# Kernel optimization log

Hardware: AMD Instinct MI355X
Metric: run time of the kernel (lower is better)

The kernel has to match this reference:

```python
import jax, jax.numpy as jnp
import numpy as np
from jax import lax

EPS = 1e-5  # torch BatchNorm default eps

# Binarization with straight-through estimator (hard-tanh gradient window),
# matching BinaryFunc in dizcza/MCMC_BinaryNet.
@jax.custom_vjp
def binarize(x):
    return jnp.sign(x)

def _bin_fwd(x):
    return jnp.sign(x), x

def _bin_bwd(res, g):
    return (g * (jnp.abs(res) <= 1.0).astype(g.dtype),)

binarize.defvjp(_bin_fwd, _bin_bwd)

def bn2d(x, gamma, beta):
    # training-mode BatchNorm2d: batch stats over (N,H,W), biased variance
    m = x.mean(axis=(0, 2, 3), keepdims=True)
    v = x.var(axis=(0, 2, 3), keepdims=True)
    xn = (x - m) * lax.rsqrt(v + EPS)
    return xn * gamma[None, :, None, None] + beta[None, :, None, None]

def bn1d(x, gamma, beta):
    m = x.mean(axis=0, keepdims=True)
    v = x.var(axis=0, keepdims=True)
    return (x - m) * lax.rsqrt(v + EPS) * gamma[None, :] + beta[None, :]

def bconv(x, w):
    # BinaryDecorator(Conv2d): sign(x) conv sign(W), padding=0, no bias
    return lax.conv_general_dilated(binarize(x), binarize(w), (1, 1), 'VALID',
                                    dimension_numbers=('NCHW', 'OIHW', 'NCHW'))

def maxpool2(x):
    return lax.reduce_window(x, -jnp.inf, lax.max, (1, 1, 2, 2), (1, 1, 2, 2), 'VALID')

def prelu(x, a):
    return jnp.where(x >= 0, x, a * x)


def setup_inputs() -> dict:
    key = jax.random.key(0)
    ks = iter(jax.random.split(key, 16))
    conv_channels = [3, 128, 256, 512]
    fc_sizes = [512 * 6 * 6, 1024, 10]
    d = {'x': jax.random.normal(next(ks), (128, 3, 64, 64), jnp.float32)}
    for i, (cin, cout) in enumerate(zip(conv_channels[:-1], conv_channels[1:])):
        d[f'cg{i}'] = jnp.ones((cin,), jnp.float32)          # BN2d gamma
        d[f'cb{i}'] = jnp.zeros((cin,), jnp.float32)         # BN2d beta
        d[f'cw{i}'] = jax.random.normal(next(ks), (cout, cin, 3, 3), jnp.float32) * 0.05
        d[f'cp{i}'] = jnp.full((1,), 0.25, jnp.float32)      # PReLU (num_parameters=1)
    for i, (fin, fout) in enumerate(zip(fc_sizes[:-1], fc_sizes[1:])):
        d[f'fg{i}'] = jnp.ones((fin,), jnp.float32)
        d[f'fb{i}'] = jnp.zeros((fin,), jnp.float32)
        d[f'fw{i}'] = jax.random.normal(next(ks), (fout, fin), jnp.float32) * 0.05
        d[f'fp{i}'] = jnp.full((1,), 0.25, jnp.float32)
    d['scale'] = jnp.full((1,), 1e-3, jnp.float32)           # ScaleLayer init
    return d


def reference(x, cg0, cb0, cw0, cp0, cg1, cb1, cw1, cp1, cg2, cb2, cw2, cp2,
              fg0, fb0, fw0, fp0, fg1, fb1, fw1, fp1, scale):
    for cg, cb, cw, cp in ((cg0, cb0, cw0, cp0), (cg1, cb1, cw1, cp1), (cg2, cb2, cw2, cp2)):
        x = bn2d(x, cg, cb)
        x = bconv(x, cw)
        x = maxpool2(x)
        x = prelu(x, cp)
    x = x.reshape(x.shape[0], -1)  # [B, 512*6*6]
    for fg, fb, fw, fp in ((fg0, fb0, fw0, fp0), (fg1, fb1, fw1, fp1)):
        x = bn1d(x, fg, fb)
        x = binarize(x) @ binarize(fw).T  # BinaryDecorator(Linear), no bias
        x = prelu(x, fp)
    return x * scale
```

## Files before the change

### kernel.cpp

```cpp
#include <hip/hip_runtime.h>
#include <cstdint>
#include <cstddef>

#define BN_EPS 1e-5


__global__ void zero_d(double* p, int n) {
  int i = blockIdx.x * blockDim.x + threadIdx.x;
  if (i < n) p[i] = 0.0;
}

__global__ void reduce_plane(const float* __restrict__ x, double* __restrict__ sums,
                             int C, int HW) {
  int c = blockIdx.x, n = blockIdx.y;
  const float* p = x + ((long)n * C + c) * HW;
  double s = 0.0, s2 = 0.0;
  for (int i = threadIdx.x; i < HW; i += blockDim.x) {
    double v = (double)p[i];
    s += v; s2 += v * v;
  }
  for (int o = 32; o > 0; o >>= 1) {
    s  += __shfl_down(s, o, 64);
    s2 += __shfl_down(s2, o, 64);
  }
  __shared__ double ls[4], ls2[4];
  int lane = threadIdx.x & 63, w = threadIdx.x >> 6;
  if (lane == 0) { ls[w] = s; ls2[w] = s2; }
  __syncthreads();
  if (threadIdx.x == 0) {
    double a = 0, b = 0;
    for (int i = 0; i < 4; i++) { a += ls[i]; b += ls2[i]; }
    atomicAdd(&sums[2 * c], a);
    atomicAdd(&sums[2 * c + 1], b);
  }
}

__global__ void reduce_cl(const float* __restrict__ x, double* __restrict__ sums,
                          int C, long rows) {
  int lane = threadIdx.x & 63, wv = threadIdx.x >> 6;
  int c = blockIdx.x * 64 + lane;
  double s = 0.0, s2 = 0.0;
  for (long r = blockIdx.y * 4 + wv; r < rows; r += (long)gridDim.y * 4) {
    double v = (double)x[r * C + c];
    s += v; s2 += v * v;
  }
  __shared__ double ls[4][64], ls2[4][64];
  ls[wv][lane] = s; ls2[wv][lane] = s2;
  __syncthreads();
  if (threadIdx.x < 64) {
    double a = ls[0][lane] + ls[1][lane] + ls[2][lane] + ls[3][lane];
    double b = ls2[0][lane] + ls2[1][lane] + ls2[2][lane] + ls2[3][lane];
    atomicAdd(&sums[2 * c], a);
    atomicAdd(&sums[2 * c + 1], b);
  }
}

__global__ void reduce_cols2(const float* __restrict__ x, double* __restrict__ sums,
                             int R, int F, int RS) {
  int f = blockIdx.x * blockDim.x + threadIdx.x;
  int r0 = blockIdx.y * RS, r1 = min(r0 + RS, R);
  double s = 0.0, s2 = 0.0;
  for (int r = r0; r < r1; r++) {
    double v = (double)x[(long)r * F + f];
    s += v; s2 += v * v;
  }
  atomicAdd(&sums[2 * f], s);
  atomicAdd(&sums[2 * f + 1], s2);
}

__global__ void finalize_stats(const double* __restrict__ sums, double2* __restrict__ st,
                               int C, double cnt) {
  int c = blockIdx.x * blockDim.x + threadIdx.x;
  if (c >= C) return;
  double m = sums[2 * c] / cnt;
  double v = sums[2 * c + 1] / cnt - m * m;
  st[c] = make_double2(m, 1.0 / sqrt(v + BN_EPS));
}


__global__ void pack_bits_c1(const float* __restrict__ x, const double2* __restrict__ st,
                             const float* __restrict__ g, const float* __restrict__ b,
                             uint64_t* __restrict__ rows) {
  int wid = blockIdx.x * 4 + (threadIdx.x >> 6);
  int lane = threadIdx.x & 63;
  int n = wid / 192, rem = wid % 192;
  int ci = rem >> 6, y = rem & 63;
  double2 s = st[ci];
  float xv = x[(((long)n * 3 + ci) * 64 + y) * 64 + lane];
  float xn = (float)(((double)xv - s.x) * s.y) * g[ci] + b[ci];
  uint64_t m = __ballot(xn > 0.f);
  if (lane == 0) rows[wid] = m;
}

__global__ void pack_wc1(const float* __restrict__ w, uint32_t* __restrict__ wm) {
  int co = threadIdx.x;
  uint32_t m = 0;
  for (int j = 0; j < 27; j++) m |= (uint32_t)(w[co * 27 + j] > 0.f) << j;
  wm[co] = m;
}

__global__ void pack_cl(const float* __restrict__ acl, const double2* __restrict__ st,
                        const float* __restrict__ g, const float* __restrict__ b,
                        uint64_t* __restrict__ out, int C, long nwords, int lw) {
  long wid = (long)blockIdx.x * 4 + (threadIdx.x >> 6);
  if (wid >= nwords) return;
  int lane = threadIdx.x & 63;
  long row = wid >> lw;
  int w = (int)(wid & ((1 << lw) - 1));
  int c = w * 64 + lane;
  double2 s = st[c];
  float xv = acl[row * C + c];
  float xn = (float)(((double)xv - s.x) * s.y) * g[c] + b[c];
  uint64_t m = __ballot(xn > 0.f);
  if (lane == 0) out[wid] = m;
}

__global__ void pack_wconv(const float* __restrict__ w, uint64_t* __restrict__ out,
                           int CO, int CI, int W) {
  int i = blockIdx.x * blockDim.x + threadIdx.x;
  int total = CO * 9 * W;
  if (i >= total) return;
  int wd = i % W;
  int t = i / W;
  int tap = t % 9, co = t / 9;
  uint64_t bits = 0;
  for (int k = 0; k < 64; k++) {
    int ci = wd * 64 + k;
    bits |= (uint64_t)(w[((long)co * CI + ci) * 9 + tap] > 0.f) << k;
  }
  out[i] = bits;
}

__global__ void pack_nz(const float* __restrict__ x, const double2* __restrict__ st,
                        const float* __restrict__ g, const float* __restrict__ b,
                        uint64_t* __restrict__ out, int R, int F) {
  int Wf = F >> 6;
  long wid = (long)blockIdx.x * 4 + (threadIdx.x >> 6);
  if (wid >= (long)R * Wf) return;
  int lane = threadIdx.x & 63;
  long r = wid / Wf;
  int w = (int)(wid % Wf);
  int f = w * 64 + lane;
  double2 s = st[f];
  double d = (double)x[r * F + f] - s.x;
  float xn = (float)(d * s.y) * g[f] + b[f];
  uint64_t sm = __ballot(xn > 0.f);
  uint64_t nm = __ballot(d != 0.0);
  if (lane == 0) { out[2 * wid] = sm; out[2 * wid + 1] = nm; }
}

__global__ void pack_wfc2(const float* __restrict__ w, uint64_t* __restrict__ out,
                          int O, int F) {
  int Wf = F >> 6;
  long wid = (long)blockIdx.x * 4 + (threadIdx.x >> 6);
  if (wid >= (long)O * Wf) return;
  int lane = threadIdx.x & 63;
  long o = wid / Wf;
  int wd = (int)(wid % Wf);
  uint64_t m = __ballot(w[o * F + wd * 64 + lane] > 0.f);
  if (lane == 0) out[wid] = m;
}


__global__ __launch_bounds__(256) void conv1_pool3(const uint64_t* __restrict__ rows,
                                                   const uint32_t* __restrict__ wm,
                                                   const float* __restrict__ cp,
                                                   float* __restrict__ out) {
  __shared__ uint64_t rL[192];
  __shared__ uint32_t wL[128];
  __shared__ uint32_t mL[61 * 4];
  int n = blockIdx.y, chunk = blockIdx.x, t = threadIdx.x;
  if (t < 192) rL[t] = rows[n * 192 + t];
  if (t < 128) wL[t] = wm[t];
  __syncthreads();
  if (t < 244) {
    int pl = t >> 2, quad = t & 3;
    int pos = chunk * 61 + pl;
    if (pos < 961) {
      int py = pos / 31, px = pos - py * 31;
      int cy = 2 * py + (quad >> 1), cx = 2 * px + (quad & 1);
      uint32_t m = 0;
#pragma unroll
      for (int ci = 0; ci < 3; ci++)
#pragma unroll
        for (int ky = 0; ky < 3; ky++)
          m |= (uint32_t)((rL[ci * 64 + cy + ky] >> cx) & 7) << (ci * 9 + ky * 3);
      mL[pl * 4 + quad] = m;
    }
  }
  __syncthreads();
  int co = t & 127, slot = t >> 7;
  float alpha = cp[0];
  uint32_t w = wL[co];
  for (int i = slot; i < 61; i += 2) {
    int pos = chunk * 61 + i;
    if (pos >= 961) break;
    int p0 = __popc(mL[4 * i] ^ w);
    int p1 = __popc(mL[4 * i + 1] ^ w);
    int p2 = __popc(mL[4 * i + 2] ^ w);
    int p3 = __popc(mL[4 * i + 3] ^ w);
    int dot = 27 - 2 * min(min(p0, p1), min(p2, p3));
    float f = (float)dot;
    out[((long)n * 961 + pos) * 128 + co] = dot >= 0 ? f : alpha * f;
  }
}

template <int W, int IH>
__device__ __forceinline__ void load_half(uint64_t (&h)[4][2 * W],
                                          const uint64_t* __restrict__ sIn,
                                          int py, int cx) {
#pragma unroll
  for (int cy = 0; cy < 4; cy++) {
    const uint64_t* p = &sIn[((2 * py + cy) * IH + cx) * W];
#pragma unroll
    for (int i = 0; i < 2 * W; i++) h[cy][i] = p[i];
  }
}

template <int W>
__device__ __forceinline__ void conv_quad(const uint64_t (&A)[4][2 * W],
                                          const uint64_t (&B)[4][2 * W],
                                          const uint64_t (&wr)[9 * W],
                                          int& a00, int& a01, int& a10, int& a11) {
  a00 = a01 = a10 = a11 = 0;
#pragma unroll
  for (int cy = 0; cy < 4; cy++) {
#pragma unroll
    for (int dy = 0; dy < 2; dy++) {
      int ky = cy - dy;
      if (ky < 0 || ky > 2) continue;
#pragma unroll
      for (int dx = 0; dx < 2; dx++) {
        int acc = 0;
#pragma unroll
        for (int kx = 0; kx < 3; kx++) {
          int col = dx + kx;
#pragma unroll
          for (int wd = 0; wd < W; wd++) {
            uint64_t pv = (col < 2) ? A[cy][col * W + wd] : B[cy][(col - 2) * W + wd];
            acc += __popcll(pv ^ wr[(ky * 3 + kx) * W + wd]);
          }
        }
        if (dy == 0) { if (dx == 0) a00 += acc; else a01 += acc; }
        else         { if (dx == 0) a10 += acc; else a11 += acc; }
      }
    }
  }
}

template <int W, int IH, int PH, int CHUNK>
__global__ __attribute__((amdgpu_flat_work_group_size(256, 256),
                          amdgpu_waves_per_eu(2, 3)))
void convp_slide(
    const uint64_t* __restrict__ in, const uint64_t* __restrict__ wt,
    const float* __restrict__ cp, float* __restrict__ out, int CO) {
  __shared__ uint64_t sIn[10 * IH * W];
  int n = blockIdx.y;
  int cg = blockIdx.x / CHUNK, chunk = blockIdx.x % CHUNK;
  int t = threadIdx.x, lane = t & 63, slot = t >> 6;
  int r0 = chunk * 8;
  int nr = min(10, IH - r0);
  const uint64_t* src = in + ((long)n * IH + r0) * (IH * W);
  for (int i = t; i < nr * IH * W; i += 256) sIn[i] = src[i];
  int co = cg * 64 + lane;
  uint64_t wr[9 * W];
  const uint64_t* wg = wt + (long)co * (9 * W);
#pragma unroll
  for (int i = 0; i < 9 * W; i++) wr[i] = wg[i];
  __syncthreads();
  int py = chunk * 4 + slot;
  if (py >= PH) return;
  float alpha = cp[0];
  const int K = 9 * 64 * W;
  uint64_t hA[4][2 * W], hB[4][2 * W];
  load_half<W, IH>(hA, sIn, slot, 0);
#pragma unroll
  for (int px = 0; px < PH; px += 2) {
    load_half<W, IH>(hB, sIn, slot, 2 * px + 2);
    {
      int a00, a01, a10, a11;
      conv_quad<W>(hA, hB, wr, a00, a01, a10, a11);
      int dot = K - 2 * min(min(a00, a01), min(a10, a11));
      float f = (float)dot;
      out[((long)n * PH * PH + py * PH + px) * CO + co] = dot >= 0 ? f : alpha * f;
    }
    if (px + 1 < PH) {
      load_half<W, IH>(hA, sIn, slot, 2 * px + 4);
      int a00, a01, a10, a11;
      conv_quad<W>(hB, hA, wr, a00, a01, a10, a11);
      int dot = K - 2 * min(min(a00, a01), min(a10, a11));
      float f = (float)dot;
      out[((long)n * PH * PH + py * PH + px + 1) * CO + co] = dot >= 0 ? f : alpha * f;
    }
  }
}

template <int W, int IH, int PH, int POSCH, bool CL>
__global__ __attribute__((amdgpu_flat_work_group_size(256, 256),
                          amdgpu_waves_per_eu(2, 3)))
void convp_pool3(
    const uint64_t* __restrict__ in, const uint64_t* __restrict__ wt,
    const float* __restrict__ cp, float* __restrict__ out, int CO) {
  __shared__ uint64_t sIn[IH * IH * W];
  int n = blockIdx.y;
  int cg = blockIdx.x / POSCH;
  int chunk = blockIdx.x % POSCH;
  int t = threadIdx.x;
  const uint64_t* src = in + (long)n * (IH * IH * W);
  for (int i = t; i < IH * IH * W; i += 256) sIn[i] = src[i];
  int lane = t & 63;
  int slot = t >> 6;
  int co = cg * 64 + lane;
  uint64_t wr[9 * W];
  const uint64_t* wg = wt + (long)co * (9 * W);
#pragma unroll
  for (int i = 0; i < 9 * W; i++) wr[i] = wg[i];
  __syncthreads();
  float alpha = cp[0];
  for (int pos = chunk * 4 + slot; pos < PH * PH; pos += POSCH * 4) {
    int py = pos / PH, px = pos % PH;
    int a00 = 0, a01 = 0, a10 = 0, a11 = 0;
#pragma unroll
    for (int cy = 0; cy < 4; cy++) {
      uint64_t row[4 * W];
      const uint64_t* rp = &sIn[((2 * py + cy) * IH + 2 * px) * W];
#pragma unroll
      for (int i = 0; i < 4 * W; i++) row[i] = rp[i];
#pragma unroll
      for (int dy = 0; dy < 2; dy++) {
        int ky = cy - dy;
        if (ky < 0 || ky > 2) continue;
#pragma unroll
        for (int dx = 0; dx < 2; dx++) {
          int a = 0;
#pragma unroll
          for (int kx = 0; kx < 3; kx++)
#pragma unroll
            for (int wd = 0; wd < W; wd++)
              a += __popcll(row[(dx + kx) * W + wd] ^ wr[(ky * 3 + kx) * W + wd]);
          if (dy == 0) { if (dx == 0) a00 += a; else a01 += a; }
          else         { if (dx == 0) a10 += a; else a11 += a; }
        }
      }
    }
    int pmin = min(min(a00, a01), min(a10, a11));
    int dot = 9 * 64 * W - 2 * pmin;
    float f = (float)dot;
    long idx = CL ? (((long)n * PH * PH + pos) * CO + co)
                  : (((long)n * CO + co) * PH * PH + pos);
    out[idx] = dot >= 0 ? f : alpha * f;
  }
}


__global__ void fc_bin(const uint64_t* __restrict__ xp, const uint64_t* __restrict__ wp,
                       const float* __restrict__ cp, float* __restrict__ out,
                       int O, int Wf) {
  __shared__ uint64_t xs[288], xz[288];
  int r = blockIdx.y;
  for (int i = threadIdx.x; i < Wf; i += blockDim.x) {
    xs[i] = xp[((long)r * Wf + i) * 2];
    xz[i] = xp[((long)r * Wf + i) * 2 + 1];
  }
  __syncthreads();
  int o = blockIdx.x * blockDim.x + threadIdx.x;
  if (o >= O) return;
  int pc = 0, nzc = 0;
  const uint64_t* wr = wp + (long)o * Wf;
  for (int wd = 0; wd < Wf; wd++) {
    uint64_t nz = xz[wd];
    pc  += __popcll((xs[wd] ^ wr[wd]) & nz);
    nzc += __popcll(nz);
  }
  int dot = nzc - 2 * pc;
  float f = (float)dot;
  float alpha = cp[0];
  out[(long)r * O + o] = dot >= 0 ? f : alpha * f;
}

__global__ void fc_bin_scale(const uint64_t* __restrict__ xp, const uint64_t* __restrict__ wp,
                             const float* __restrict__ cp, const float* __restrict__ scale,
                             float* __restrict__ out, int R, int O, int Wf) {
  int i = blockIdx.x * blockDim.x + threadIdx.x;
  if (i >= R * O) return;
  int o = i % O, r = i / O;
  int pc = 0, nzc = 0;
  for (int wd = 0; wd < Wf; wd++) {
    uint64_t nz = xp[((long)r * Wf + wd) * 2 + 1];
    pc  += __popcll((xp[((long)r * Wf + wd) * 2] ^ wp[(long)o * Wf + wd]) & nz);
    nzc += __popcll(nz);
  }
  int dot = nzc - 2 * pc;
  float f = (float)dot;
  float alpha = cp[0];
  f = dot >= 0 ? f : alpha * f;
  out[i] = f * scale[0];
}


extern "C" void kernel_launch(void* const* d_in, const int* in_sizes, int n_in,
                              void* d_out, int out_size, void* d_ws, size_t ws_size,
                              hipStream_t stream) {
  const float* x   = (const float*)d_in[0];
  const float* cg0 = (const float*)d_in[1];
  const float* cb0 = (const float*)d_in[2];
  const float* cw0 = (const float*)d_in[3];
  const float* cp0 = (const float*)d_in[4];
  const float* cg1 = (const float*)d_in[5];
  const float* cb1 = (const float*)d_in[6];
  const float* cw1 = (const float*)d_in[7];
  const float* cp1 = (const float*)d_in[8];
  const float* cg2 = (const float*)d_in[9];
  const float* cb2 = (const float*)d_in[10];
  const float* cw2 = (const float*)d_in[11];
  const float* cp2 = (const float*)d_in[12];
  const float* fg0 = (const float*)d_in[13];
  const float* fb0 = (const float*)d_in[14];
  const float* fw0 = (const float*)d_in[15];
  const float* fp0 = (const float*)d_in[16];
  const float* fg1 = (const float*)d_in[17];
  const float* fb1 = (const float*)d_in[18];
  const float* fw1 = (const float*)d_in[19];
  const float* fp1 = (const float*)d_in[20];
  const float* scl = (const float*)d_in[21];

  char* ws = (char*)d_ws;
  size_t off = 0;
  auto alloc = [&](size_t bytes) {
    size_t r = off;
    off += (bytes + 255) & ~(size_t)255;
    return r;
  };
  const int C0_OFF = 0, C1_OFF = 16, C2_OFF = 160, C3_OFF = 448, C4_OFF = 18944;
  const int NCH = 19968;

  double*   sums  = (double*)(ws + alloc((size_t)NCH * 2 * sizeof(double)));
  double2*  stats = (double2*)(ws + alloc((size_t)NCH * sizeof(double2)));
  uint64_t* rows0 = (uint64_t*)(ws + alloc(128L * 3 * 64 * 8));
  uint32_t* wm1   = (uint32_t*)(ws + alloc(128L * 4));
  float*    a1    = (float*)(ws + alloc(128L * 961 * 128 * 4));
  uint64_t* s1p   = (uint64_t*)(ws + alloc(128L * 961 * 2 * 8));
  uint64_t* w1p   = (uint64_t*)(ws + alloc(256L * 9 * 2 * 8));
  float*    a2    = (float*)(ws + alloc(128L * 196 * 256 * 4));
  uint64_t* s2p   = (uint64_t*)(ws + alloc(128L * 196 * 4 * 8));
  uint64_t* w2p   = (uint64_t*)(ws + alloc(512L * 9 * 4 * 8));
  float*    a3    = (float*)(ws + alloc(128L * 512 * 36 * 4));
  uint64_t* s3p   = (uint64_t*)(ws + alloc(128L * 288 * 2 * 8));
  uint64_t* w3p   = (uint64_t*)(ws + alloc(1024L * 288 * 8));
  float*    f1    = (float*)(ws + alloc(128L * 1024 * 4));
  uint64_t* s4p   = (uint64_t*)(ws + alloc(128L * 16 * 2 * 8));
  uint64_t* w4p   = (uint64_t*)(ws + alloc(10L * 16 * 8));

  const int B = 256;

  zero_d<<<dim3(156), B, 0, stream>>>(sums, NCH * 2);

  reduce_plane<<<dim3(3, 128), B, 0, stream>>>(x, sums + 2 * C0_OFF, 3, 4096);
  finalize_stats<<<1, 64, 0, stream>>>(sums + 2 * C0_OFF, stats + C0_OFF, 3, 524288.0);
  pack_bits_c1<<<dim3(6144), B, 0, stream>>>(x, stats + C0_OFF, cg0, cb0, rows0);
  pack_wc1<<<1, 128, 0, stream>>>(cw0, wm1);
  conv1_pool3<<<dim3(16, 128), B, 0, stream>>>(rows0, wm1, cp0, a1);

  reduce_cl<<<dim3(2, 256), B, 0, stream>>>(a1, sums + 2 * C1_OFF, 128, 123008L);
  finalize_stats<<<1, 128, 0, stream>>>(sums + 2 * C1_OFF, stats + C1_OFF, 128, 123008.0);
  pack_cl<<<dim3(61504), B, 0, stream>>>(a1, stats + C1_OFF, cg1, cb1, s1p, 128, 246016L, 1);
  pack_wconv<<<dim3(18), B, 0, stream>>>(cw1, w1p, 256, 128, 2);
  convp_slide<2, 31, 14, 4><<<dim3(16, 128), B, 0, stream>>>(s1p, w1p, cp1, a2, 256);

  reduce_cl<<<dim3(4, 128), B, 0, stream>>>(a2, sums + 2 * C2_OFF, 256, 25088L);
  finalize_stats<<<1, 256, 0, stream>>>(sums + 2 * C2_OFF, stats + C2_OFF, 256, 25088.0);
  pack_cl<<<dim3(25088), B, 0, stream>>>(a2, stats + C2_OFF, cg2, cb2, s2p, 256, 100352L, 2);
  pack_wconv<<<dim3(72), B, 0, stream>>>(cw2, w2p, 512, 256, 4);
  convp_pool3<4, 14, 6, 2, false><<<dim3(16, 128), B, 0, stream>>>(s2p, w2p, cp2, a3, 512);

  reduce_cols2<<<dim3(72, 8), B, 0, stream>>>(a3, sums + 2 * C3_OFF, 128, 18432, 16);
  finalize_stats<<<dim3(72), B, 0, stream>>>(sums + 2 * C3_OFF, stats + C3_OFF, 18432, 128.0);
  pack_nz<<<dim3(9216), B, 0, stream>>>(a3, stats + C3_OFF, fg0, fb0, s3p, 128, 18432);
  pack_wfc2<<<dim3(73728), B, 0, stream>>>(fw0, w3p, 1024, 18432);
  fc_bin<<<dim3(4, 128), B, 0, stream>>>(s3p, w3p, fp0, f1, 1024, 288);

  reduce_cols2<<<dim3(4, 8), B, 0, stream>>>(f1, sums + 2 * C4_OFF, 128, 1024, 16);
  finalize_stats<<<dim3(4), B, 0, stream>>>(sums + 2 * C4_OFF, stats + C4_OFF, 1024, 128.0);
  pack_nz<<<dim3(512), B, 0, stream>>>(f1, stats + C4_OFF, fg1, fb1, s4p, 128, 1024);
  pack_wfc2<<<dim3(40), B, 0, stream>>>(fw1, w4p, 10, 1024);
  fc_bin_scale<<<dim3(5), B, 0, stream>>>(s4p, w4p, fp1, scl, (float*)d_out, 128, 10, 16);
}
```

Baseline: 530.4 us.

## Unify binary conv kernels into streaming form and batch FC rows with transposed weights

Replaces the sliding-window and pool3 binary conv kernels with one streaming kernel. It loads each input word once and scatters its popcounts into all four pooled accumulators, and raises waves_per_eu to 4. The FC layer now takes transposed packed weights for coalesced reads and processes four batch rows per block to reuse each weight word. Per-row nonzero counts are precomputed with atomics in pack_nz instead of inside the FC loop. The changes trade more register pressure and atomic traffic for fewer shared-memory loads and less weight bandwidth.

New measurement: 674.9 us. +27.2%, slower.

```diff
diff --git a/kernel.cpp b/kernel.cpp
--- a/kernel.cpp
+++ b/kernel.cpp
@@ -133,7 +133,8 @@
 
 __global__ void pack_nz(const float* __restrict__ x, const double2* __restrict__ st,
                         const float* __restrict__ g, const float* __restrict__ b,
-                        uint64_t* __restrict__ out, int R, int F) {
+                        uint64_t* __restrict__ out, double* __restrict__ nzc,
+                        int R, int F) {
   int Wf = F >> 6;
   long wid = (long)blockIdx.x * 4 + (threadIdx.x >> 6);
   if (wid >= (long)R * Wf) return;
@@ -146,11 +147,14 @@
   float xn = (float)(d * s.y) * g[f] + b[f];
   uint64_t sm = __ballot(xn > 0.f);
   uint64_t nm = __ballot(d != 0.0);
-  if (lane == 0) { out[2 * wid] = sm; out[2 * wid + 1] = nm; }
-}
-
-__global__ void pack_wfc2(const float* __restrict__ w, uint64_t* __restrict__ out,
-                          int O, int F) {
+  if (lane == 0) {
+    out[2 * wid] = sm; out[2 * wid + 1] = nm;
+    atomicAdd(&nzc[r], (double)__popcll(nm));
+  }
+}
+
+__global__ void pack_wfc2_t(const float* __restrict__ w, uint64_t* __restrict__ out,
+                            int O, int F) {
   int Wf = F >> 6;
   long wid = (long)blockIdx.x * 4 + (threadIdx.x >> 6);
   if (wid >= (long)O * Wf) return;
@@ -158,7 +162,7 @@
   long o = wid / Wf;
   int wd = (int)(wid % Wf);
   uint64_t m = __ballot(w[o * F + wd * 64 + lane] > 0.f);
-  if (lane == 0) out[wid] = m;
+  if (lane == 0) out[(long)wd * O + o] = m;
 }
 
 
@@ -205,55 +209,11 @@
   }
 }
 
-template <int W, int IH>
-__device__ __forceinline__ void load_half(uint64_t (&h)[4][2 * W],
-                                          const uint64_t* __restrict__ sIn,
-                                          int py, int cx) {
-#pragma unroll
-  for (int cy = 0; cy < 4; cy++) {
-    const uint64_t* p = &sIn[((2 * py + cy) * IH + cx) * W];
-#pragma unroll
-    for (int i = 0; i < 2 * W; i++) h[cy][i] = p[i];
-  }
-}
-
-template <int W>
-__device__ __forceinline__ void conv_quad(const uint64_t (&A)[4][2 * W],
-                                          const uint64_t (&B)[4][2 * W],
-                                          const uint64_t (&wr)[9 * W],
-                                          int& a00, int& a01, int& a10, int& a11) {
-  a00 = a01 = a10 = a11 = 0;
-#pragma unroll
-  for (int cy = 0; cy < 4; cy++) {
-#pragma unroll
-    for (int dy = 0; dy < 2; dy++) {
-      int ky = cy - dy;
-      if (ky < 0 || ky > 2) continue;
-#pragma unroll
-      for (int dx = 0; dx < 2; dx++) {
-        int acc = 0;
-#pragma unroll
-        for (int kx = 0; kx < 3; kx++) {
-          int col = dx + kx;
-#pragma unroll
-          for (int wd = 0; wd < W; wd++) {
-            uint64_t pv = (col < 2) ? A[cy][col * W + wd] : B[cy][(col - 2) * W + wd];
-            acc += __popcll(pv ^ wr[(ky * 3 + kx) * W + wd]);
-          }
-        }
-        if (dy == 0) { if (dx == 0) a00 += acc; else a01 += acc; }
-        else         { if (dx == 0) a10 += acc; else a11 += acc; }
-      }
-    }
-  }
-}
-
-template <int W, int IH, int PH, int CHUNK>
+template <int W, int IH, int PH, int CHUNK, bool CL>
 __global__ __attribute__((amdgpu_flat_work_group_size(256, 256),
-                          amdgpu_waves_per_eu(2, 3)))
-void convp_slide(
-    const uint64_t* __restrict__ in, const uint64_t* __restrict__ wt,
-    const float* __restrict__ cp, float* __restrict__ out, int CO) {
+                          amdgpu_waves_per_eu(2, 4)))
+void convp_stream(const uint64_t* __restrict__ in, const uint64_t* __restrict__ wt,
+                  const float* __restrict__ cp, float* __restrict__ out, int CO) {
   __shared__ uint64_t sIn[10 * IH * W];
   int n = blockIdx.y;
   int cg = blockIdx.x / CHUNK, chunk = blockIdx.x % CHUNK;
@@ -272,125 +232,86 @@
   if (py >= PH) return;
   float alpha = cp[0];
   const int K = 9 * 64 * W;
-  uint64_t hA[4][2 * W], hB[4][2 * W];
-  load_half<W, IH>(hA, sIn, slot, 0);
-#pragma unroll
-  for (int px = 0; px < PH; px += 2) {
-    load_half<W, IH>(hB, sIn, slot, 2 * px + 2);
-    {
-      int a00, a01, a10, a11;
-      conv_quad<W>(hA, hB, wr, a00, a01, a10, a11);
-      int dot = K - 2 * min(min(a00, a01), min(a10, a11));
-      float f = (float)dot;
-      out[((long)n * PH * PH + py * PH + px) * CO + co] = dot >= 0 ? f : alpha * f;
-    }
-    if (px + 1 < PH) {
-      load_half<W, IH>(hA, sIn, slot, 2 * px + 4);
-      int a00, a01, a10, a11;
-      conv_quad<W>(hB, hA, wr, a00, a01, a10, a11);
-      int dot = K - 2 * min(min(a00, a01), min(a10, a11));
-      float f = (float)dot;
-      out[((long)n * PH * PH + py * PH + px + 1) * CO + co] = dot >= 0 ? f : alpha * f;
-    }
-  }
-}
-
-template <int W, int IH, int PH, int POSCH, bool CL>
-__global__ __attribute__((amdgpu_flat_work_group_size(256, 256),
-                          amdgpu_waves_per_eu(2, 3)))
-void convp_pool3(
-    const uint64_t* __restrict__ in, const uint64_t* __restrict__ wt,
-    const float* __restrict__ cp, float* __restrict__ out, int CO) {
-  __shared__ uint64_t sIn[IH * IH * W];
-  int n = blockIdx.y;
-  int cg = blockIdx.x / POSCH;
-  int chunk = blockIdx.x % POSCH;
-  int t = threadIdx.x;
-  const uint64_t* src = in + (long)n * (IH * IH * W);
-  for (int i = t; i < IH * IH * W; i += 256) sIn[i] = src[i];
-  int lane = t & 63;
-  int slot = t >> 6;
-  int co = cg * 64 + lane;
-  uint64_t wr[9 * W];
-  const uint64_t* wg = wt + (long)co * (9 * W);
-#pragma unroll
-  for (int i = 0; i < 9 * W; i++) wr[i] = wg[i];
-  __syncthreads();
-  float alpha = cp[0];
-  for (int pos = chunk * 4 + slot; pos < PH * PH; pos += POSCH * 4) {
-    int py = pos / PH, px = pos % PH;
+  const uint64_t* base = &sIn[(2 * slot) * (IH * W)];
+#pragma unroll
+  for (int px = 0; px < PH; px++) {
     int a00 = 0, a01 = 0, a10 = 0, a11 = 0;
 #pragma unroll
     for (int cy = 0; cy < 4; cy++) {
-      uint64_t row[4 * W];
-      const uint64_t* rp = &sIn[((2 * py + cy) * IH + 2 * px) * W];
-#pragma unroll
-      for (int i = 0; i < 4 * W; i++) row[i] = rp[i];
-#pragma unroll
-      for (int dy = 0; dy < 2; dy++) {
-        int ky = cy - dy;
-        if (ky < 0 || ky > 2) continue;
-#pragma unroll
-        for (int dx = 0; dx < 2; dx++) {
-          int a = 0;
-#pragma unroll
-          for (int kx = 0; kx < 3; kx++)
-#pragma unroll
-            for (int wd = 0; wd < W; wd++)
-              a += __popcll(row[(dx + kx) * W + wd] ^ wr[(ky * 3 + kx) * W + wd]);
-          if (dy == 0) { if (dx == 0) a00 += a; else a01 += a; }
-          else         { if (dx == 0) a10 += a; else a11 += a; }
+#pragma unroll
+      for (int col = 0; col < 4; col++) {
+#pragma unroll
+        for (int wd = 0; wd < W; wd++) {
+          uint64_t v = base[(cy * IH + 2 * px + col) * W + wd];
+#pragma unroll
+          for (int dy = 0; dy < 2; dy++) {
+            int ky = cy - dy;
+            if (ky < 0 || ky > 2) continue;
+#pragma unroll
+            for (int dx = 0; dx < 2; dx++) {
+              int kx = col - dx;
+              if (kx < 0 || kx > 2) continue;
+              int p = __popcll(v ^ wr[(ky * 3 + kx) * W + wd]);
+              if (dy == 0) { if (dx == 0) a00 += p; else a01 += p; }
+              else         { if (dx == 0) a10 += p; else a11 += p; }
+            }
+          }
         }
       }
     }
-    int pmin = min(min(a00, a01), min(a10, a11));
-    int dot = 9 * 64 * W - 2 * pmin;
+    int dot = K - 2 * min(min(a00, a01), min(a10, a11));
     float f = (float)dot;
-    long idx = CL ? (((long)n * PH * PH + pos) * CO + co)
-                  : (((long)n * CO + co) * PH * PH + pos);
+    long idx = CL ? (((long)n * PH * PH + py * PH + px) * CO + co)
+                  : (((long)n * CO + co) * PH * PH + (py * PH + px));
     out[idx] = dot >= 0 ? f : alpha * f;
   }
 }
 
 
-__global__ void fc_bin(const uint64_t* __restrict__ xp, const uint64_t* __restrict__ wp,
-                       const float* __restrict__ cp, float* __restrict__ out,
-                       int O, int Wf) {
-  __shared__ uint64_t xs[288], xz[288];
-  int r = blockIdx.y;
-  for (int i = threadIdx.x; i < Wf; i += blockDim.x) {
-    xs[i] = xp[((long)r * Wf + i) * 2];
-    xz[i] = xp[((long)r * Wf + i) * 2 + 1];
+__global__ void fc_bin4(const uint64_t* __restrict__ xp, const uint64_t* __restrict__ wp_t,
+                        const double* __restrict__ nzc, const float* __restrict__ cp,
+                        float* __restrict__ out, int O, int Wf) {
+  __shared__ uint64_t xs[4][288], xz[4][288];
+  int r0 = blockIdx.y * 4;
+  for (int i = threadIdx.x; i < 4 * Wf; i += blockDim.x) {
+    int rr = i / Wf, wd = i - rr * Wf;
+    xs[rr][wd] = xp[(((long)(r0 + rr)) * Wf + wd) * 2];
+    xz[rr][wd] = xp[(((long)(r0 + rr)) * Wf + wd) * 2 + 1];
   }
   __syncthreads();
   int o = blockIdx.x * blockDim.x + threadIdx.x;
   if (o >= O) return;
-  int pc = 0, nzc = 0;
-  const uint64_t* wr = wp + (long)o * Wf;
+  int pc0 = 0, pc1 = 0, pc2 = 0, pc3 = 0;
   for (int wd = 0; wd < Wf; wd++) {
-    uint64_t nz = xz[wd];
-    pc  += __popcll((xs[wd] ^ wr[wd]) & nz);
-    nzc += __popcll(nz);
-  }
-  int dot = nzc - 2 * pc;
-  float f = (float)dot;
+    uint64_t w = wp_t[(long)wd * O + o];
+    pc0 += __popcll((xs[0][wd] ^ w) & xz[0][wd]);
+    pc1 += __popcll((xs[1][wd] ^ w) & xz[1][wd]);
+    pc2 += __popcll((xs[2][wd] ^ w) & xz[2][wd]);
+    pc3 += __popcll((xs[3][wd] ^ w) & xz[3][wd]);
+  }
   float alpha = cp[0];
-  out[(long)r * O + o] = dot >= 0 ? f : alpha * f;
-}
-
-__global__ void fc_bin_scale(const uint64_t* __restrict__ xp, const uint64_t* __restrict__ wp,
-                             const float* __restrict__ cp, const float* __restrict__ scale,
-                             float* __restrict__ out, int R, int O, int Wf) {
+  int dots[4] = {pc0, pc1, pc2, pc3};
+#pragma unroll
+  for (int rr = 0; rr < 4; rr++) {
+    int dot = (int)nzc[r0 + rr] - 2 * dots[rr];
+    float f = (float)dot;
+    out[(long)(r0 + rr) * O + o] = dot >= 0 ? f : alpha * f;
+  }
+}
+
+__global__ void fc_bin_scale(const uint64_t* __restrict__ xp, const uint64_t* __restrict__ wp_t,
+                             const double* __restrict__ nzc, const float* __restrict__ cp,
+                             const float* __restrict__ scale, float* __restrict__ out,
+                             int R, int O, int Wf) {
   int i = blockIdx.x * blockDim.x + threadIdx.x;
   if (i >= R * O) return;
   int o = i % O, r = i / O;
-  int pc = 0, nzc = 0;
+  int pc = 0;
   for (int wd = 0; wd < Wf; wd++) {
     uint64_t nz = xp[((long)r * Wf + wd) * 2 + 1];
-    pc  += __popcll((xp[((long)r * Wf + wd) * 2] ^ wp[(long)o * Wf + wd]) & nz);
-    nzc += __popcll(nz);
-  }
-  int dot = nzc - 2 * pc;
+    pc += __popcll((xp[((long)r * Wf + wd) * 2] ^ wp_t[(long)wd * O + o]) & nz);
+  }
+  int dot = (int)nzc[r] - 2 * pc;
   float f = (float)dot;
   float alpha = cp[0];
   f = dot >= 0 ? f : alpha * f;
@@ -435,6 +356,8 @@
   const int NCH = 19968;
 
   double*   sums  = (double*)(ws + alloc((size_t)NCH * 2 * sizeof(double)));
+  double*   nzcA  = (double*)(ws + alloc(128 * sizeof(double)));
+  double*   nzcB  = (double*)(ws + alloc(128 * sizeof(double)));
   double2*  stats = (double2*)(ws + alloc((size_t)NCH * sizeof(double2)));
   uint64_t* rows0 = (uint64_t*)(ws + alloc(128L * 3 * 64 * 8));
   uint32_t* wm1   = (uint32_t*)(ws + alloc(128L * 4));
@@ -453,7 +376,7 @@
 
   const int B = 256;
 
-  zero_d<<<dim3(156), B, 0, stream>>>(sums, NCH * 2);
+  zero_d<<<dim3(157), B, 0, stream>>>(sums, NCH * 2 + 256);
 
   reduce_plane<<<dim3(3, 128), B, 0, stream>>>(x, sums + 2 * C0_OFF, 3, 4096);
   finalize_stats<<<1, 64, 0, stream>>>(sums + 2 * C0_OFF, stats + C0_OFF, 3, 524288.0);
@@ -465,23 +388,23 @@
   finalize_stats<<<1, 128, 0, stream>>>(sums + 2 * C1_OFF, stats + C1_OFF, 128, 123008.0);
   pack_cl<<<dim3(61504), B, 0, stream>>>(a1, stats + C1_OFF, cg1, cb1, s1p, 128, 246016L, 1);
   pack_wconv<<<dim3(18), B, 0, stream>>>(cw1, w1p, 256, 128, 2);
-  convp_slide<2, 31, 14, 4><<<dim3(16, 128), B, 0, stream>>>(s1p, w1p, cp1, a2, 256);
+  convp_stream<2, 31, 14, 4, true><<<dim3(16, 128), B, 0, stream>>>(s1p, w1p, cp1, a2, 256);
 
   reduce_cl<<<dim3(4, 128), B, 0, stream>>>(a2, sums + 2 * C2_OFF, 256, 25088L);
   finalize_stats<<<1, 256, 0, stream>>>(sums + 2 * C2_OFF, stats + C2_OFF, 256, 25088.0);
   pack_cl<<<dim3(25088), B, 0, stream>>>(a2, stats + C2_OFF, cg2, cb2, s2p, 256, 100352L, 2);
   pack_wconv<<<dim3(72), B, 0, stream>>>(cw2, w2p, 512, 256, 4);
-  convp_pool3<4, 14, 6, 2, false><<<dim3(16, 128), B, 0, stream>>>(s2p, w2p, cp2, a3, 512);
+  convp_stream<4, 14, 6, 2, false><<<dim3(16, 128), B, 0, stream>>>(s2p, w2p, cp2, a3, 512);
 
   reduce_cols2<<<dim3(72, 8), B, 0, stream>>>(a3, sums + 2 * C3_OFF, 128, 18432, 16);
   finalize_stats<<<dim3(72), B, 0, stream>>>(sums + 2 * C3_OFF, stats + C3_OFF, 18432, 128.0);
-  pack_nz<<<dim3(9216), B, 0, stream>>>(a3, stats + C3_OFF, fg0, fb0, s3p, 128, 18432);
-  pack_wfc2<<<dim3(73728), B, 0, stream>>>(fw0, w3p, 1024, 18432);
-  fc_bin<<<dim3(4, 128), B, 0, stream>>>(s3p, w3p, fp0, f1, 1024, 288);
+  pack_nz<<<dim3(9216), B, 0, stream>>>(a3, stats + C3_OFF, fg0, fb0, s3p, nzcA, 128, 18432);
+  pack_wfc2_t<<<dim3(73728), B, 0, stream>>>(fw0, w3p, 1024, 18432);
+  fc_bin4<<<dim3(4, 32), B, 0, stream>>>(s3p, w3p, nzcA, fp0, f1, 1024, 288);
 
   reduce_cols2<<<dim3(4, 8), B, 0, stream>>>(f1, sums + 2 * C4_OFF, 128, 1024, 16);
   finalize_stats<<<dim3(4), B, 0, stream>>>(sums + 2 * C4_OFF, stats + C4_OFF, 1024, 128.0);
-  pack_nz<<<dim3(512), B, 0, stream>>>(f1, stats + C4_OFF, fg1, fb1, s4p, 128, 1024);
-  pack_wfc2<<<dim3(40), B, 0, stream>>>(fw1, w4p, 10, 1024);
-  fc_bin_scale<<<dim3(5), B, 0, stream>>>(s4p, w4p, fp1, scl, (float*)d_out, 128, 10, 16);
-}
+  pack_nz<<<dim3(512), B, 0, stream>>>(f1, stats + C4_OFF, fg1, fb1, s4p, nzcB, 128, 1024);
+  pack_wfc2_t<<<dim3(40), B, 0, stream>>>(fw1, w4p, 10, 1024);
+  fc_bin_scale<<<dim3(5), B, 0, stream>>>(s4p, w4p, nzcB, fp1, scl, (float*)d_out, 128, 10, 16);
+}
```
